# Optimization experiments

Hardware: AMD Instinct MI355X
Metric: run time of the kernel (lower is better)

## Reference

```python
import jax, jax.numpy as jnp
import numpy as np
import math

H = 1024
NH = 16
D = H // NH  # 64
EPS = 1e-5


def _layernorm(x, g, b):
    mu = jnp.mean(x, axis=-1, keepdims=True)
    var = jnp.mean(jnp.square(x - mu), axis=-1, keepdims=True)
    return (x - mu) * jax.lax.rsqrt(var + EPS) * g + b


def setup_inputs() -> dict:
    key = jax.random.key(0)
    ks = jax.random.split(key, 12)
    B, T = 2, 2048
    q = jax.random.normal(ks[0], (B, T, H), jnp.float32)
    k = jax.random.normal(ks[1], (B, T, H), jnp.float32)
    v = jax.random.normal(ks[2], (B, T, H), jnp.float32)
    pad_mask = jax.random.randint(ks[3], (B, T), 0, 2) > 0
    s = 0.02
    Wq = jax.random.normal(ks[4], (H, H), jnp.float32) * s
    Wk = jax.random.normal(ks[5], (H, H), jnp.float32) * s
    Wv = jax.random.normal(ks[6], (H, H), jnp.float32) * s
    Wo = jax.random.normal(ks[7], (H, H), jnp.float32) * s
    W1 = jax.random.normal(ks[8], (4 * H, H), jnp.float32) * s
    b1 = jnp.zeros((4 * H,), jnp.float32)
    W2 = jax.random.normal(ks[9], (H, 4 * H), jnp.float32) * s
    b2 = jnp.zeros((H,), jnp.float32)
    g1 = jnp.ones((H,), jnp.float32); be1 = jnp.zeros((H,), jnp.float32)
    g2 = jnp.ones((H,), jnp.float32); be2 = jnp.zeros((H,), jnp.float32)
    return dict(q=q, k=k, v=v, pad_mask=pad_mask, Wq=Wq, Wk=Wk, Wv=Wv, Wo=Wo,
                W1=W1, b1=b1, W2=W2, b2=b2, g1=g1, be1=be1, g2=g2, be2=be2)


def reference(q, k, v, pad_mask, Wq, Wk, Wv, Wo, W1, b1, W2, b2, g1, be1, g2, be2):
    B, Tq, _ = q.shape
    Tv = v.shape[1]
    # torch nn.Linear: x @ W.T
    Q = (q @ Wq.T).reshape(B, NH, Tq, D)  # faithful to torch .view head split
    K = (k @ Wk.T).reshape(B, NH, Tv, D)
    V = (v @ Wv.T).reshape(B, NH, Tv, D)
    logits = jnp.einsum('baih,bajh->baij', Q, K)  # [B,NH,Tq,Tv]
    neg_inf = jnp.float32(-jnp.inf)
    logits = jnp.where(pad_mask[:, None, None, :], logits, neg_inf)
    attn = jax.nn.softmax(logits / math.sqrt(D), axis=-1)
    # post-softmax query-mask multiply (custom)
    attn = attn * pad_mask[:, None, :, None].astype(attn.dtype)
    h = jnp.einsum('baij,bajh->baih', attn, V).reshape(B, Tq, H)
    h = h @ Wo.T
    h = _layernorm(q + h, g1, be1)
    ff = jax.nn.gelu(h @ W1.T + b1, approximate=False) @ W2.T + b2  # dropout = identity (eval)
    return _layernorm(h + ff, g2, be2)
```

## Files before the change

kernel.cpp:

```cpp
#include <hip/hip_runtime.h>

typedef unsigned short u16;
typedef unsigned int u32;
typedef __attribute__((ext_vector_type(8))) __bf16 bf16x8;
typedef __attribute__((ext_vector_type(4))) float f32x4;
typedef __attribute__((ext_vector_type(16))) float f32x16;
typedef __attribute__((ext_vector_type(4))) unsigned short u16x4;
typedef __attribute__((ext_vector_type(8))) unsigned short u16x8;

#define LOG2E 1.44269504088896340736f

__device__ __forceinline__ u16 f2bf(float f) {
  union { float f; unsigned u; } c; c.f = f;
  unsigned r = c.u + 0x7FFFu + ((c.u >> 16) & 1u);
  return (u16)(r >> 16);
}
__device__ __forceinline__ float bf2f(u16 h) {
  union { unsigned u; float f; } c; c.u = ((unsigned)h) << 16;
  return c.f;
}

__device__ __forceinline__ void gload_lds16(const u16* g, u16* l) {
  __builtin_amdgcn_global_load_lds((const __attribute__((address_space(1))) unsigned int*)g,
                                   (__attribute__((address_space(3))) unsigned int*)l, 16, 0, 0);
}

__global__ __launch_bounds__(256) void cvt_all(
    const float* __restrict__ s0, const float* __restrict__ s1, const float* __restrict__ s2,
    const float* __restrict__ s3, const float* __restrict__ s4, const float* __restrict__ s5,
    const float* __restrict__ s6, const float* __restrict__ s7, const float* __restrict__ s8,
    u16* __restrict__ d0, u16* __restrict__ d1, u16* __restrict__ d2,
    u16* __restrict__ d3, u16* __restrict__ d4, u16* __restrict__ d5,
    u16* __restrict__ d6, u16* __restrict__ d7, u16* __restrict__ d8) {
  int i = blockIdx.x * 256 + threadIdx.x;
  if (i >= 6291456) return;
  const float* src; u16* dst; int off;
  if (i < 3145728) {
    if (i < 1048576)      { src = s0; dst = d0; off = 0; }
    else if (i < 2097152) { src = s1; dst = d1; off = 1048576; }
    else                  { src = s2; dst = d2; off = 2097152; }
  } else if (i < 4194304) {
    if (i < 3407872)      { src = s3; dst = d3; off = 3145728; }
    else if (i < 3670016) { src = s4; dst = d4; off = 3407872; }
    else if (i < 3932160) { src = s5; dst = d5; off = 3670016; }
    else                  { src = s6; dst = d6; off = 3932160; }
  } else {
    if (i < 5242880)      { src = s7; dst = d7; off = 4194304; }
    else                  { src = s8; dst = d8; off = 5242880; }
  }
  int j = i - off;
  f32x4 v = ((const f32x4*)src)[j];
  u16x4 o;
  o[0] = f2bf(v[0]); o[1] = f2bf(v[1]); o[2] = f2bf(v[2]); o[3] = f2bf(v[3]);
  ((u16x4*)dst)[j] = o;
}

__global__ void build_masks(const void* __restrict__ pm, float* __restrict__ maskbias,
                            float* __restrict__ qmask, int n) {
  __shared__ int sflag;
  if (threadIdx.x == 0) sflag = 0;
  __syncthreads();
  const unsigned* pw = (const unsigned*)pm;
  int nwords = n / 4;
  int local = 0;
  for (int i = threadIdx.x; i < nwords; i += blockDim.x)
    if (pw[i] > 1u) local = 1;
  if (local) atomicOr(&sflag, 1);
  __syncthreads();
  bool isbool = (sflag != 0);
  for (int i = threadIdx.x; i < n; i += blockDim.x) {
    int m = isbool ? (int)((const unsigned char*)pm)[i] : ((const int*)pm)[i];
    maskbias[i] = m ? 0.0f : -2e30f;
    qmask[i]    = m ? 1.0f : 0.0f;
  }
}

template<int EPI>
__device__ __forceinline__ void gemm_core(const u16* __restrict__ A, const u16* __restrict__ Bw,
                                          const float* __restrict__ bias, u16* __restrict__ C,
                                          int N, int Kstride, int Klen, int bn, int bm, int tid) {
  __shared__ u16 As[128 * 32];
  __shared__ u16 Bs[128 * 32];
  int wave = tid >> 6, lane = tid & 63;
  int l15 = lane & 15, l4 = lane >> 4;
  int wr = (wave >> 1) * 64, wc = (wave & 1) * 64;
  int mrow0 = bm * 128, ncol0 = bn * 128;
  int srow = lane >> 2;
  int scol = (lane & 3) * 8;

  f32x4 acc[4][4];
#pragma unroll
  for (int i = 0; i < 4; i++)
#pragma unroll
    for (int j = 0; j < 4; j++) acc[i][j] = (f32x4)0.0f;

  for (int k0 = 0; k0 < Klen; k0 += 32) {
#pragma unroll
    for (int c = 0; c < 2; c++) {
      int q = wave * 2 + c;
      gload_lds16(A  + (size_t)(mrow0 + q * 16 + srow) * Kstride + k0 + scol, &As[q * 512]);
      gload_lds16(Bw + (size_t)(ncol0 + q * 16 + srow) * Kstride + k0 + scol, &Bs[q * 512]);
    }
    __syncthreads();
    bf16x8 af[4], bfr[4];
#pragma unroll
    for (int mi = 0; mi < 4; mi++) af[mi]  = *(const bf16x8*)(&As[(wr + mi * 16 + l15) * 32 + l4 * 8]);
#pragma unroll
    for (int ni = 0; ni < 4; ni++) bfr[ni] = *(const bf16x8*)(&Bs[(wc + ni * 16 + l15) * 32 + l4 * 8]);
#pragma unroll
    for (int mi = 0; mi < 4; mi++)
#pragma unroll
      for (int ni = 0; ni < 4; ni++)
        acc[mi][ni] = __builtin_amdgcn_mfma_f32_16x16x32_bf16(af[mi], bfr[ni], acc[mi][ni], 0, 0, 0);
    __syncthreads();
  }

#pragma unroll
  for (int ni = 0; ni < 4; ni++) {
    int gcol = ncol0 + wc + ni * 16 + l15;
    float bv = (EPI > 0) ? bias[gcol] : 0.0f;
#pragma unroll
    for (int mi = 0; mi < 4; mi++) {
#pragma unroll
      for (int r = 0; r < 4; r++) {
        int grow = mrow0 + wr + mi * 16 + l4 * 4 + r;
        float v = acc[mi][ni][r] + bv;
        if (EPI == 2) v = 0.5f * v * (1.0f + erff(v * 0.70710678118654752f));
        C[(size_t)grow * N + gcol] = f2bf(v);
      }
    }
  }
}

template<int EPI>
__global__ __launch_bounds__(256) void gemm_bt(const u16* __restrict__ A, const u16* __restrict__ Bw,
                                               const float* __restrict__ bias, u16* __restrict__ C,
                                               int N, int K) {
  gemm_core<EPI>(A, Bw, bias, C, N, K, K, blockIdx.x, blockIdx.y, threadIdx.x);
}

__global__ __launch_bounds__(256) void gemm_splitk(const u16* __restrict__ A, const u16* __restrict__ Bw,
                                                   u16* __restrict__ P, int N, int Kstride, int Kc) {
  int z = blockIdx.z;
  size_t M = (size_t)gridDim.y * 128;
  gemm_core<0>(A + (size_t)z * Kc, Bw + (size_t)z * Kc, nullptr,
               P + (size_t)z * M * N, N, Kstride, Kc, blockIdx.x, blockIdx.y, threadIdx.x);
}

__global__ __launch_bounds__(256) void gemm_qkv(const u16* __restrict__ qb, const u16* __restrict__ kb,
                                                const u16* __restrict__ vb,
                                                const u16* __restrict__ wq, const u16* __restrict__ wk,
                                                const u16* __restrict__ wv,
                                                u16* __restrict__ Qo, u16* __restrict__ Ko, u16* __restrict__ Vo) {
  const u16* A; const u16* W; u16* C;
  if (blockIdx.z == 0)      { A = qb; W = wq; C = Qo; }
  else if (blockIdx.z == 1) { A = kb; W = wk; C = Ko; }
  else                      { A = vb; W = wv; C = Vo; }
  gemm_core<0>(A, W, nullptr, C, 1024, 1024, 1024, blockIdx.x, blockIdx.y, threadIdx.x);
}

__global__ __launch_bounds__(256) void transpose64(const u16* __restrict__ in, u16* __restrict__ out) {
  int bh = blockIdx.y, tb = blockIdx.x;
  __shared__ u16 tile[64 * 72];
  int tid = threadIdx.x;
#pragma unroll
  for (int it = 0; it < 2; it++) {
    int idx = it * 256 + tid;
    int r = idx >> 3, c8 = (idx & 7) * 8;
    u16x8 v = *(const u16x8*)(in + ((size_t)bh * 2048 + tb * 64 + r) * 64 + c8);
    int byte = ((r * 72 + c8) * 2) ^ (((r >> 3) & 7) << 4);
    *(u16x8*)((char*)tile + byte) = v;
  }
  __syncthreads();
#pragma unroll
  for (int it = 0; it < 2; it++) {
    int idx = it * 256 + tid;
    int d = idx >> 3, t8 = (idx & 7) * 8;
    u16x8 o;
#pragma unroll
    for (int e = 0; e < 8; e++) {
      int t = t8 + e;
      int byte = ((t * 72 + d) * 2) ^ (((t >> 3) & 7) << 4);
      o[e] = *(const u16*)((const char*)tile + byte);
    }
    *(u16x8*)(out + ((size_t)bh * 64 + d) * 2048 + tb * 64 + t8) = o;
  }
}

__global__ __launch_bounds__(256, 4) void attn4(const u16* __restrict__ Q, const u16* __restrict__ Kg,
                                                const u16* __restrict__ VT,
                                                const float* __restrict__ maskbias,
                                                u16* __restrict__ O0, u16* __restrict__ O1,
                                                float* __restrict__ Ms, float* __restrict__ Ss) {
  const int T = 2048;
  int bh = blockIdx.x;
  int qt = blockIdx.y;
  int sp = blockIdx.z;
  int b = bh >> 4;
  const u16* Qh = Q  + (size_t)bh * T * 64;
  const u16* Kh = Kg + (size_t)bh * T * 64;
  const u16* Vh = VT + (size_t)bh * T * 64;
  u16* Oh = (sp ? O1 : O0) + (size_t)bh * T * 64;
  const float* mb = maskbias + b * T + sp * 1024;
  int tid = threadIdx.x, w = tid >> 6, l = tid & 63;
  int q32 = l & 31, h = l >> 5;
  int qbase = qt * 128 + w * 32;
  const float C = 0.125f * LOG2E;

  __shared__ u16 Ks[2][4096];
  __shared__ u16 Vs[2][4096];

  bf16x8 qf[4];
#pragma unroll
  for (int dc = 0; dc < 4; dc++)
    qf[dc] = *(const bf16x8*)(Qh + (size_t)(qbase + q32) * 64 + dc * 16 + h * 8);

  int rl = l >> 3, ob = (l & 7) * 16;
  int osw = ob ^ (rl << 4);
  int r0 = w * 16 + rl, r1 = w * 16 + 8 + rl;
  const u16* pK0 = Kh + (size_t)(sp * 1024 + r0) * 64 + (osw >> 1);
  const u16* pK1 = Kh + (size_t)(sp * 1024 + r1) * 64 + (osw >> 1);
  const u16* pV0 = Vh + (size_t)r0 * 2048 + sp * 1024 + (osw >> 1);
  const u16* pV1 = Vh + (size_t)r1 * 2048 + sp * 1024 + (osw >> 1);
  u16* dK0 = &Ks[0][0] + (w * 16) * 64;
  u16* dK1 = &Ks[0][0] + (w * 16 + 8) * 64;
  u16* dV0 = &Vs[0][0] + (w * 16) * 64;
  u16* dV1 = &Vs[0][0] + (w * 16 + 8) * 64;

  auto stage = [&](int buf) {
    gload_lds16(pK0, dK0 + buf * 4096);
    gload_lds16(pK1, dK1 + buf * 4096);
    gload_lds16(pV0, dV0 + buf * 4096);
    gload_lds16(pV1, dV1 + buf * 4096);
    pK0 += 4096; pK1 += 4096; pV0 += 64; pV1 += 64;
  };

  f32x16 acc[2];
  acc[0] = (f32x16)0.0f; acc[1] = (f32x16)0.0f;
  float m_ = -3e30f, s_ = 0.0f;

  int swz = (q32 & 7) << 4;

  stage(0);
  for (int t = 0; t < 16; t++) {
    int cur = t & 1;
    __syncthreads();
    if (t < 15) stage(cur ^ 1);
    const char* ksb = (const char*)(&Ks[0][0] + cur * 4096);
    const char* vsb = (const char*)(&Vs[0][0] + cur * 4096);

    bf16x8 kf[2][4];
#pragma unroll
    for (int kvc = 0; kvc < 2; kvc++)
#pragma unroll
      for (int dc = 0; dc < 4; dc++)
        kf[kvc][dc] = *(const bf16x8*)(ksb + (kvc * 32 + q32) * 128 + ((dc * 32 + h * 16) ^ swz));

    f32x16 st[2];
    st[0] = (f32x16)0.0f; st[1] = (f32x16)0.0f;
#pragma unroll
    for (int kvc = 0; kvc < 2; kvc++)
#pragma unroll
      for (int dc = 0; dc < 4; dc++)
        st[kvc] = __builtin_amdgcn_mfma_f32_32x32x16_bf16(kf[kvc][dc], qf[dc], st[kvc], 0, 0, 0);

    float p[32];
    float pmax = -3e30f;
#pragma unroll
    for (int kvc = 0; kvc < 2; kvc++) {
#pragma unroll
      for (int g = 0; g < 4; g++) {
        f32x4 mv = *(const f32x4*)(mb + t * 64 + kvc * 32 + g * 8 + h * 4);
#pragma unroll
        for (int r = 0; r < 4; r++) {
          float val = st[kvc][g * 4 + r] * C + mv[r];
          p[kvc * 16 + g * 4 + r] = val;
          pmax = fmaxf(pmax, val);
        }
      }
    }
    pmax = fmaxf(pmax, __shfl_xor(pmax, 32));

    if (__any(pmax - m_ > 8.0f)) {
      float mnew = fmaxf(m_, pmax);
      float fsc = __builtin_amdgcn_exp2f(m_ - mnew);
      s_ *= fsc;
      m_ = mnew;
#pragma unroll
      for (int g = 0; g < 4; g++)
#pragma unroll
        for (int r = 0; r < 4; r++) {
          float f = __shfl(fsc, g * 8 + h * 4 + r);
          acc[0][g * 4 + r] *= f;
          acc[1][g * 4 + r] *= f;
        }
    }

    float rsum = 0.0f;
    u32 wds[16];
#pragma unroll
    for (int i = 0; i < 16; i++) {
      float a = __builtin_amdgcn_exp2f(p[2 * i] - m_);
      float bq = __builtin_amdgcn_exp2f(p[2 * i + 1] - m_);
      rsum += a + bq;
      union { __bf16 h2[2]; u32 u; } cv;
      cv.h2[0] = (__bf16)a; cv.h2[1] = (__bf16)bq;
      wds[i] = cv.u;
    }
    rsum += __shfl_xor(rsum, 32);
    s_ += rsum;

#pragma unroll
    for (int kvc = 0; kvc < 2; kvc++) {
      int bse = kvc * 8;
      u32 sw0 = __shfl_xor(wds[bse + 0], 32), sw1 = __shfl_xor(wds[bse + 1], 32);
      u32 sw2 = __shfl_xor(wds[bse + 2], 32), sw3 = __shfl_xor(wds[bse + 3], 32);
      u32 sw4 = __shfl_xor(wds[bse + 4], 32), sw5 = __shfl_xor(wds[bse + 5], 32);
      u32 sw6 = __shfl_xor(wds[bse + 6], 32), sw7 = __shfl_xor(wds[bse + 7], 32);
      union { u32 u[4]; bf16x8 v; } pa0, pa1;
      pa0.u[0] = h ? sw2 : wds[bse + 0];
      pa0.u[1] = h ? sw3 : wds[bse + 1];
      pa0.u[2] = h ? wds[bse + 2] : sw0;
      pa0.u[3] = h ? wds[bse + 3] : sw1;
      pa1.u[0] = h ? sw6 : wds[bse + 4];
      pa1.u[1] = h ? sw7 : wds[bse + 5];
      pa1.u[2] = h ? wds[bse + 6] : sw4;
      pa1.u[3] = h ? wds[bse + 7] : sw5;
#pragma unroll
      for (int cl = 0; cl < 2; cl++) {
        bf16x8 pa = cl ? pa1.v : pa0.v;
        int cg = kvc * 2 + cl;
#pragma unroll
        for (int dblk = 0; dblk < 2; dblk++) {
          bf16x8 vf = *(const bf16x8*)(vsb + (dblk * 32 + q32) * 128 + ((cg * 32 + h * 16) ^ swz));
          acc[dblk] = __builtin_amdgcn_mfma_f32_32x32x16_bf16(pa, vf, acc[dblk], 0, 0, 0);
        }
      }
    }
  }

#pragma unroll
  for (int g = 0; g < 4; g++) {
#pragma unroll
    for (int r = 0; r < 4; r++) {
      int row = g * 8 + h * 4 + r;
#pragma unroll
      for (int dblk = 0; dblk < 2; dblk++)
        Oh[(size_t)(qbase + row) * 64 + dblk * 32 + q32] = f2bf(acc[dblk][g * 4 + r]);
    }
  }
  if (h == 0) {
    int ro = sp * 65536 + bh * 2048 + qbase + q32;
    Ms[ro] = m_;
    Ss[ro] = s_;
  }
}

__global__ __launch_bounds__(256) void attn_combine(const u16* __restrict__ O0, const u16* __restrict__ O1,
                                                    const float* __restrict__ Ms, const float* __restrict__ Ss,
                                                    const float* __restrict__ qmaskf, u16* __restrict__ out) {
  int idx = blockIdx.x * 256 + threadIdx.x;
  int row = idx >> 3;
  int d8 = (idx & 7) * 8;
  int bh = row >> 11, r = row & 2047, b = bh >> 4;
  float m0 = Ms[row], m1 = Ms[65536 + row];
  float mstar = fmaxf(m0, m1);
  float w0 = __builtin_amdgcn_exp2f(m0 - mstar);
  float w1 = __builtin_amdgcn_exp2f(m1 - mstar);
  float den = w0 * Ss[row] + w1 * Ss[65536 + row];
  float scale = qmaskf[b * 2048 + r] / den;
  size_t base = (size_t)row * 64 + d8;
  u16x8 a0 = *(const u16x8*)(O0 + base);
  u16x8 a1 = *(const u16x8*)(O1 + base);
  u16x8 o;
#pragma unroll
  for (int e = 0; e < 8; e++)
    o[e] = f2bf((w0 * bf2f(a0[e]) + w1 * bf2f(a1[e])) * scale);
  *(u16x8*)(out + base) = o;
}

template<int NP, int A_F32, int ADD_BIAS, int OUT_F32>
__global__ __launch_bounds__(256) void add_ln_multi(const void* __restrict__ Ap,
                                                    const u16* __restrict__ P0, const u16* __restrict__ P1,
                                                    const u16* __restrict__ P2, const u16* __restrict__ P3,
                                                    const float* __restrict__ bias,
                                                    const float* __restrict__ g, const float* __restrict__ be,
                                                    void* __restrict__ outp) {
  int row = blockIdx.x, tid = threadIdx.x;
  int lane = tid & 63, wave = tid >> 6;
  size_t rb = (size_t)row * 1024;
  float x[4];
  if (A_F32) {
    f32x4 a = ((const f32x4*)((const float*)Ap + rb))[tid];
#pragma unroll
    for (int j = 0; j < 4; j++) x[j] = a[j];
  } else {
    u16x4 au = ((const u16x4*)((const u16*)Ap + rb))[tid];
#pragma unroll
    for (int j = 0; j < 4; j++) x[j] = bf2f(au[j]);
  }
  {
    u16x4 p = ((const u16x4*)(P0 + rb))[tid];
#pragma unroll
    for (int j = 0; j < 4; j++) x[j] += bf2f(p[j]);
  }
  if (NP > 1) {
    u16x4 p = ((const u16x4*)(P1 + rb))[tid];
#pragma unroll
    for (int j = 0; j < 4; j++) x[j] += bf2f(p[j]);
  }
  if (NP > 2) {
    u16x4 p = ((const u16x4*)(P2 + rb))[tid];
#pragma unroll
    for (int j = 0; j < 4; j++) x[j] += bf2f(p[j]);
  }
  if (NP > 3) {
    u16x4 p = ((const u16x4*)(P3 + rb))[tid];
#pragma unroll
    for (int j = 0; j < 4; j++) x[j] += bf2f(p[j]);
  }
  if (ADD_BIAS) {
    f32x4 bv = ((const f32x4*)bias)[tid];
#pragma unroll
    for (int j = 0; j < 4; j++) x[j] += bv[j];
  }
  float s = x[0] + x[1] + x[2] + x[3];
  float q = x[0] * x[0] + x[1] * x[1] + x[2] * x[2] + x[3] * x[3];
#pragma unroll
  for (int m = 1; m < 64; m <<= 1) { s += __shfl_xor(s, m); q += __shfl_xor(q, m); }
  __shared__ float rs[4], rq[4];
  if (lane == 0) { rs[wave] = s; rq[wave] = q; }
  __syncthreads();
  float S = rs[0] + rs[1] + rs[2] + rs[3];
  float Qq = rq[0] + rq[1] + rq[2] + rq[3];
  float mean = S * (1.0f / 1024.0f);
  float var = Qq * (1.0f / 1024.0f) - mean * mean;
  float rstd = rsqrtf(var + 1e-5f);
  if (OUT_F32) {
    f32x4 y;
#pragma unroll
    for (int j = 0; j < 4; j++) { int col = tid * 4 + j; y[j] = (x[j] - mean) * rstd * g[col] + be[col]; }
    ((f32x4*)((float*)outp + rb))[tid] = y;
  } else {
    u16x4 y;
#pragma unroll
    for (int j = 0; j < 4; j++) { int col = tid * 4 + j; y[j] = f2bf((x[j] - mean) * rstd * g[col] + be[col]); }
    ((u16x4*)((u16*)outp + rb))[tid] = y;
  }
}

extern "C" void kernel_launch(void* const* d_in, const int* in_sizes, int n_in,
                              void* d_out, int out_size, void* d_ws, size_t ws_size,
                              hipStream_t stream) {
  const float* q   = (const float*)d_in[0];
  const float* k   = (const float*)d_in[1];
  const float* v   = (const float*)d_in[2];
  const void*  pad = d_in[3];
  const float* Wq  = (const float*)d_in[4];
  const float* Wk  = (const float*)d_in[5];
  const float* Wv  = (const float*)d_in[6];
  const float* Wo  = (const float*)d_in[7];
  const float* W1  = (const float*)d_in[8];
  const float* b1  = (const float*)d_in[9];
  const float* W2  = (const float*)d_in[10];
  const float* b2  = (const float*)d_in[11];
  const float* g1  = (const float*)d_in[12];
  const float* be1 = (const float*)d_in[13];
  const float* g2  = (const float*)d_in[14];
  const float* be2 = (const float*)d_in[15];
  float* out = (float*)d_out;
  char* ws = (char*)d_ws;
  const size_t MB = 1u << 20;

  u16* wq_b = (u16*)(ws + 0 * MB);
  u16* wk_b = (u16*)(ws + 2 * MB);
  u16* wv_b = (u16*)(ws + 4 * MB);
  u16* wo_b = (u16*)(ws + 6 * MB);
  u16* w1_b = (u16*)(ws + 8 * MB);
  u16* w2_b = (u16*)(ws + 16 * MB);
  u16* qb   = (u16*)(ws + 24 * MB);
  u16* kb   = (u16*)(ws + 32 * MB);
  u16* vb   = (u16*)(ws + 40 * MB);
  u16* Qb   = (u16*)(ws + 48 * MB);
  u16* Kb   = (u16*)(ws + 56 * MB);
  u16* Vb   = (u16*)(ws + 64 * MB);
  u16* VTb  = (u16*)(ws + 72 * MB);
  u16* hatt = (u16*)(ws + 80 * MB);
  u16* Op0  = (u16*)(ws + 24 * MB);
  u16* Op1  = (u16*)(ws + 32 * MB);
  float* Ms = (float*)(ws + 88 * MB);
  float* Ss = (float*)(ws + 89 * MB);
  u16* WP   = (u16*)(ws + 40 * MB);
  u16* h1b  = (u16*)(ws + 24 * MB);
  u16* ff1  = (u16*)(ws + 32 * MB);
  u16* Fp   = (u16*)(ws + 64 * MB);
  float* maskbias = (float*)(ws + 96 * MB);
  float* qmaskf   = (float*)(ws + 96 * MB + 16384);

  build_masks<<<1, 256, 0, stream>>>(pad, maskbias, qmaskf, in_sizes[3]);

  cvt_all<<<24576, 256, 0, stream>>>(q, k, v, Wq, Wk, Wv, Wo, W1, W2,
                                     qb, kb, vb, wq_b, wk_b, wv_b, wo_b, w1_b, w2_b);

  gemm_qkv<<<dim3(8, 32, 3), 256, 0, stream>>>(qb, kb, vb, wq_b, wk_b, wv_b, Qb, Kb, Vb);

  transpose64<<<dim3(32, 32), 256, 0, stream>>>(Vb, VTb);

  attn4<<<dim3(32, 16, 2), 256, 0, stream>>>(Qb, Kb, VTb, maskbias, Op0, Op1, Ms, Ss);

  attn_combine<<<2048, 256, 0, stream>>>(Op0, Op1, Ms, Ss, qmaskf, hatt);

  gemm_splitk<<<dim3(8, 32, 2), 256, 0, stream>>>(hatt, wo_b, WP, 1024, 1024, 512);

  add_ln_multi<2, 1, 0, 0><<<4096, 256, 0, stream>>>(q, WP, WP + 4194304, nullptr, nullptr,
                                                     nullptr, g1, be1, h1b);

  gemm_bt<2><<<dim3(32, 32), 256, 0, stream>>>(h1b, w1_b, b1, ff1, 4096, 1024);

  gemm_splitk<<<dim3(8, 32, 4), 256, 0, stream>>>(ff1, w2_b, Fp, 1024, 4096, 1024);

  add_ln_multi<4, 0, 1, 1><<<4096, 256, 0, stream>>>(h1b, Fp, Fp + 4194304, Fp + 2 * 4194304,
                                                     Fp + 3 * 4194304, b2, g2, be2, out);
}
```

Before: 313.1 us.

## Double-buffer GEMM LDS loads, stage epilogue through LDS, use fast GELU

```diff
diff --git a/kernel.cpp b/kernel.cpp
--- a/kernel.cpp
+++ b/kernel.cpp
@@ -23,6 +23,17 @@
 __device__ __forceinline__ void gload_lds16(const u16* g, u16* l) {
   __builtin_amdgcn_global_load_lds((const __attribute__((address_space(1))) unsigned int*)g,
                                    (__attribute__((address_space(3))) unsigned int*)l, 16, 0, 0);
+}
+
+__device__ __forceinline__ float gelu_fast(float x) {
+  float z = fabsf(x) * 0.70710678118654752f;
+  float t = 1.0f / (1.0f + 0.3275911f * z);
+  float poly = t * (0.254829592f + t * (-0.284496736f + t * (1.421413741f +
+               t * (-1.453152027f + t * 1.061405429f))));
+  float e = __builtin_amdgcn_exp2f(-z * z * LOG2E);
+  float erfz = 1.0f - poly * e;
+  float s = (x >= 0.0f) ? erfz : -erfz;
+  return 0.5f * x * (1.0f + s);
 }
 
 __global__ __launch_bounds__(256) void cvt_all(
@@ -79,8 +90,7 @@
 __device__ __forceinline__ void gemm_core(const u16* __restrict__ A, const u16* __restrict__ Bw,
                                           const float* __restrict__ bias, u16* __restrict__ C,
                                           int N, int Kstride, int Klen, int bn, int bm, int tid) {
-  __shared__ u16 As[128 * 32];
-  __shared__ u16 Bs[128 * 32];
+  __shared__ u16 smem[2][8192];
   int wave = tid >> 6, lane = tid & 63;
   int l15 = lane & 15, l4 = lane >> 4;
   int wr = (wave >> 1) * 64, wc = (wave & 1) * 64;
@@ -88,46 +98,74 @@
   int srow = lane >> 2;
   int scol = (lane & 3) * 8;
 
+  const u16* asrc0 = A  + (size_t)(mrow0 + (wave * 2 + 0) * 16 + srow) * Kstride + scol;
+  const u16* asrc1 = A  + (size_t)(mrow0 + (wave * 2 + 1) * 16 + srow) * Kstride + scol;
+  const u16* bsrc0 = Bw + (size_t)(ncol0 + (wave * 2 + 0) * 16 + srow) * Kstride + scol;
+  const u16* bsrc1 = Bw + (size_t)(ncol0 + (wave * 2 + 1) * 16 + srow) * Kstride + scol;
+  u16* ad0 = &smem[0][(wave * 2 + 0) * 512];
+  u16* ad1 = &smem[0][(wave * 2 + 1) * 512];
+  u16* bd0 = &smem[0][4096 + (wave * 2 + 0) * 512];
+  u16* bd1 = &smem[0][4096 + (wave * 2 + 1) * 512];
+
+  auto stage = [&](int buf, int k0) {
+    gload_lds16(asrc0 + k0, ad0 + buf * 8192);
+    gload_lds16(asrc1 + k0, ad1 + buf * 8192);
+    gload_lds16(bsrc0 + k0, bd0 + buf * 8192);
+    gload_lds16(bsrc1 + k0, bd1 + buf * 8192);
+  };
+
   f32x4 acc[4][4];
 #pragma unroll
   for (int i = 0; i < 4; i++)
 #pragma unroll
     for (int j = 0; j < 4; j++) acc[i][j] = (f32x4)0.0f;
 
-  for (int k0 = 0; k0 < Klen; k0 += 32) {
-#pragma unroll
-    for (int c = 0; c < 2; c++) {
-      int q = wave * 2 + c;
-      gload_lds16(A  + (size_t)(mrow0 + q * 16 + srow) * Kstride + k0 + scol, &As[q * 512]);
-      gload_lds16(Bw + (size_t)(ncol0 + q * 16 + srow) * Kstride + k0 + scol, &Bs[q * 512]);
-    }
+  int nsteps = Klen >> 5;
+  stage(0, 0);
+  for (int s = 0; s < nsteps; s++) {
+    int cur = s & 1;
     __syncthreads();
+    if (s + 1 < nsteps) stage(cur ^ 1, (s + 1) << 5);
+    const u16* as = &smem[cur][0];
+    const u16* bs = &smem[cur][4096];
     bf16x8 af[4], bfr[4];
 #pragma unroll
-    for (int mi = 0; mi < 4; mi++) af[mi]  = *(const bf16x8*)(&As[(wr + mi * 16 + l15) * 32 + l4 * 8]);
-#pragma unroll
-    for (int ni = 0; ni < 4; ni++) bfr[ni] = *(const bf16x8*)(&Bs[(wc + ni * 16 + l15) * 32 + l4 * 8]);
+    for (int mi = 0; mi < 4; mi++) af[mi]  = *(const bf16x8*)(as + (wr + mi * 16 + l15) * 32 + l4 * 8);
+#pragma unroll
+    for (int ni = 0; ni < 4; ni++) bfr[ni] = *(const bf16x8*)(bs + (wc + ni * 16 + l15) * 32 + l4 * 8);
 #pragma unroll
     for (int mi = 0; mi < 4; mi++)
 #pragma unroll
       for (int ni = 0; ni < 4; ni++)
         acc[mi][ni] = __builtin_amdgcn_mfma_f32_16x16x32_bf16(af[mi], bfr[ni], acc[mi][ni], 0, 0, 0);
+  }
+
+  u16* ct = &smem[0][0];
+  for (int p = 0; p < 2; p++) {
     __syncthreads();
-  }
-
-#pragma unroll
-  for (int ni = 0; ni < 4; ni++) {
-    int gcol = ncol0 + wc + ni * 16 + l15;
-    float bv = (EPI > 0) ? bias[gcol] : 0.0f;
-#pragma unroll
-    for (int mi = 0; mi < 4; mi++) {
-#pragma unroll
-      for (int r = 0; r < 4; r++) {
-        int grow = mrow0 + wr + mi * 16 + l4 * 4 + r;
-        float v = acc[mi][ni][r] + bv;
-        if (EPI == 2) v = 0.5f * v * (1.0f + erff(v * 0.70710678118654752f));
-        C[(size_t)grow * N + gcol] = f2bf(v);
+    if ((wave >> 1) == p) {
+#pragma unroll
+      for (int ni = 0; ni < 4; ni++) {
+        int gcol = ncol0 + wc + ni * 16 + l15;
+        float bv = (EPI > 0) ? bias[gcol] : 0.0f;
+#pragma unroll
+        for (int mi = 0; mi < 4; mi++) {
+#pragma unroll
+          for (int r = 0; r < 4; r++) {
+            float v = acc[mi][ni][r] + bv;
+            if (EPI == 2) v = gelu_fast(v);
+            ct[(mi * 16 + l4 * 4 + r) * 136 + wc + ni * 16 + l15] = f2bf(v);
+          }
+        }
       }
+    }
+    __syncthreads();
+    int lrow = tid >> 2, cq = tid & 3;
+#pragma unroll
+    for (int j = 0; j < 4; j++) {
+      int col = cq * 8 + j * 32;
+      u16x8 vv = *(const u16x8*)(ct + lrow * 136 + col);
+      *(u16x8*)(C + (size_t)(mrow0 + p * 64 + lrow) * N + ncol0 + col) = vv;
     }
   }
 }
```

Result: no change. 307.2 us (-1.9%).
